# Kernel optimization log

Hardware: AMD Instinct MI355X
Metric: run time of the kernel (lower is better)

The kernel has to match this reference:

```python
import jax, jax.numpy as jnp
import numpy as np

TOPK = 13
NUM_CLASSES = 80
ALPHA = 1.0
BETA = 3.0
EPS = 1e-9
K_NEAR = 4
N_BINS = 36  # theta bins: arange(0, 360, 10)


def _dist_max_per_bin(anc_points, gt_pts):
    """gt_pts: (bs,nm,360,2), anc_points: (na,2) -> (bs,nm,na,36) ray targets."""
    d = gt_pts[:, :, None, :, :] - anc_points[None, None, :, None, :]  # (bs,nm,na,360,2)
    dist = jnp.sqrt(jnp.sum(d * d, axis=-1))                           # (bs,nm,na,360)
    ang = jnp.rad2deg(jnp.arctan2(d[..., 1], d[..., 0])) % 360.0       # (bs,nm,na,360)
    theta = jnp.arange(0, 360, 360 // N_BINS).astype(ang.dtype)        # (36,)

    def per_theta(th):
        diff = jnp.abs(ang - th)
        diff = jnp.where(diff > 180.0, 360.0 - diff, diff)
        neg_v, idx = jax.lax.top_k(-diff, K_NEAR)   # 4 nearest-angle contour pts
        val = -neg_v
        dk = jnp.take_along_axis(dist, idx, axis=-1)
        dk = jnp.where(jnp.min(val, axis=-1, keepdims=True) > 3.0, 1e-6, dk)
        return jnp.max(dk, axis=-1)                 # (bs,nm,na)

    dm = jax.lax.map(per_theta, theta)              # (36,bs,nm,na); chunked to bound memory
    return jnp.maximum(jnp.moveaxis(dm, 0, -1), 1e-6)


def _mask_iou(target, pred):
    l_max = jnp.maximum(target, pred)
    l_min = jnp.maximum(jnp.minimum(target, pred), 1e-6)
    return jnp.sum(l_min, -1) / jnp.sum(l_max, -1)


def _forward(pd_scores, pd_bboxes, anc_points, gt_labels, gt_bboxes, mask_gt, gt_coor):
    bs, na, nc = pd_scores.shape
    nm = gt_bboxes.shape[1]
    gl = gt_labels[..., 0]            # (bs,nm) int
    mgt = mask_gt[..., 0]             # (bs,nm) float
    gt_pts = gt_coor.reshape(bs, nm, 360, 2)

    # select_candidates_in_gts: anchor center strictly inside gt box
    lt, rb = gt_bboxes[..., :2], gt_bboxes[..., 2:]
    deltas = jnp.concatenate([anc_points[None, None] - lt[:, :, None],
                              rb[:, :, None] - anc_points[None, None]], axis=-1)
    mask_in_gts = (jnp.min(deltas, -1) > 1e-9).astype(pd_scores.dtype)  # (bs,nm,na)
    mask_sel = (mask_in_gts * mgt[:, :, None]) > 0

    # get_box_metrics_polar (dense over (bs,nm,na) instead of boolean-mask select)
    dist_max = _dist_max_per_bin(anc_points, gt_pts)                    # (bs,nm,na,36)
    overlaps = jnp.where(mask_sel, _mask_iou(dist_max, pd_bboxes[:, None]), 0.0)
    bbox_scores = jnp.take_along_axis(jnp.swapaxes(pd_scores, 1, 2), gl[:, :, None], axis=1)
    bbox_scores = jnp.where(mask_sel, bbox_scores, 0.0)
    align_metric = (bbox_scores ** ALPHA) * (overlaps ** BETA)

    # select_topk_candidates
    _, topk_idxs = jax.lax.top_k(align_metric, TOPK)
    topk_idxs = jnp.where(mgt[:, :, None] > 0, topk_idxs, 0)
    count = jnp.sum(jax.nn.one_hot(topk_idxs, na, dtype=align_metric.dtype), axis=-2)
    mask_topk = jnp.where(count > 1, 0.0, count)
    mask_pos = mask_topk * mask_in_gts * mgt[:, :, None]

    # select_highest_overlaps
    fg = jnp.sum(mask_pos, -2)                                          # (bs,na)
    multi = fg[:, None, :] > 1
    is_max = jnp.moveaxis(jax.nn.one_hot(jnp.argmax(overlaps, 1), nm, dtype=mask_pos.dtype), -1, 1)
    mask_pos = jnp.where(multi, is_max, mask_pos)
    fg_mask = jnp.sum(mask_pos, -2)
    target_gt_idx = jnp.argmax(mask_pos, -2)                            # (bs,na)

    # per-positive ray-distance targets + polar centerness (dense, masked)
    mask_pos_b = mask_pos > 0
    gt_dist = jnp.where(mask_pos_b[..., None], dist_max, 0.0)           # (bs,nm,na,36)
    cent = jnp.sqrt(jnp.min(dist_max, -1) / jnp.max(dist_max, -1))
    centerness_gt = jnp.where(mask_pos_b, cent, 0.0)                    # (bs,nm,na)

    # get_targets
    target_labels = jnp.maximum(jnp.take_along_axis(gl, target_gt_idx, axis=1), 0)
    target_bboxes = jnp.take_along_axis(gt_bboxes, target_gt_idx[..., None], axis=1)
    target_scores = jax.nn.one_hot(target_labels, NUM_CLASSES, dtype=pd_scores.dtype)
    target_scores = jnp.where((fg_mask > 0)[..., None], target_scores, 0.0)

    am = align_metric * mask_pos
    pos_align = jnp.max(am, -1, keepdims=True)
    pos_ov = jnp.max(overlaps * mask_pos, -1, keepdims=True)
    norm_align = jnp.max(am * pos_ov / (pos_align + EPS), -2)[..., None]  # (bs,na,1)
    target_scores = target_scores * norm_align

    return (target_labels, target_bboxes, target_scores, mask_pos_b,
            target_gt_idx, gt_dist, centerness_gt, fg_mask > 0)


def setup_inputs():
    key = jax.random.key(0)
    k = jax.random.split(key, 6)
    bs, nc, nm = 2, 80, 10
    pts, strs = [], []
    for s in (8, 16, 32):  # 640x640 YOLO grid -> 8400 anchors
        n = 640 // s
        yv, xv = np.meshgrid(np.arange(n), np.arange(n), indexing='ij')
        pts.append(np.stack([(xv + 0.5) * s, (yv + 0.5) * s], -1).reshape(-1, 2))
        strs.append(np.full((pts[-1].shape[0], 1), s, dtype=np.float32))
    anc_points = jnp.asarray(np.concatenate(pts).astype(np.float32))
    stride_tensor = jnp.asarray(np.concatenate(strs))
    na = anc_points.shape[0]
    pd_scores = jax.random.uniform(k[0], (bs, na, nc), dtype=jnp.float32)
    pd_bboxes = jax.random.uniform(k[1], (bs, na, 36), dtype=jnp.float32) * 100.0 + 1.0
    gt_labels = jax.random.randint(k[2], (bs, nm, 1), 0, nc)
    ctr = jax.random.uniform(k[3], (bs, nm, 2), dtype=jnp.float32) * 440.0 + 100.0
    wh = jax.random.uniform(k[4], (bs, nm, 2), dtype=jnp.float32) * 140.0 + 40.0
    gt_bboxes = jnp.concatenate([ctr - wh / 2.0, ctr + wh / 2.0], -1)
    th = jnp.arange(360.0) * (jnp.pi / 180.0)
    rad = (jnp.min(wh, -1, keepdims=True) / 2.0) * (0.6 + 0.4 * jax.random.uniform(k[5], (bs, nm, 360), dtype=jnp.float32))
    ray = jnp.stack([jnp.cos(th), jnp.sin(th)], -1)  # (360,2)
    gt_coor = (ctr[:, :, None, :] + rad[..., None] * ray[None, None]).reshape(bs, nm, 720)
    mask_gt = jnp.ones((bs, nm, 1), dtype=jnp.float32).at[1, 7:].set(0.0)
    return dict(pd_scores=pd_scores, pd_bboxes=pd_bboxes, anc_points=anc_points,
                gt_labels=gt_labels, gt_bboxes=gt_bboxes, mask_gt=mask_gt,
                gt_coor=gt_coor, stride_tensor=stride_tensor, ss=640,
                gt_center=ctr, imgsz=640)


def reference(pd_scores, pd_bboxes, anc_points, gt_labels, gt_bboxes, mask_gt, gt_coor, stride_tensor, ss, gt_center, imgsz):
    # ss, gt_center, imgsz, stride_tensor are accepted (as in the torch signature) but unused
    return _forward(pd_scores, pd_bboxes, anc_points, gt_labels, gt_bboxes, mask_gt, gt_coor)
```

## Files before the change

### kernel.cpp

```cpp
#include <hip/hip_runtime.h>

#define BS 2
#define NM 10
#define NA 8400
#define NC 80
#define NBIN 36
#define KTOP 13
#define NRECT (BS*NM*3)
#define WDIST_CAP 16384

typedef unsigned long long ull;

__device__ __forceinline__ void rect_one(int bm, int lv,
    const float* __restrict__ gtb, const float* __restrict__ mgt,
    int& x0, int& y0, int& cx, int& cy, int& cnt, int& n, int& base){
  cnt = 0; x0 = 0; y0 = 0; cx = 0; cy = 0; n = 0; base = 0;
  if (mgt[bm] > 0.f){
    float s = (float)(8 << lv);
    n = 640 >> (3 + lv);
    base = (lv == 0) ? 0 : ((lv == 1) ? 6400 : 8000);
    float lx = gtb[bm*4+0], ly = gtb[bm*4+1];
    float rx = gtb[bm*4+2], ry = gtb[bm*4+3];
    int a0 = (int)ceilf(lx/s - 0.5f); a0 = min(max(a0, 0), n);
    while (a0 > 0   &&  (((a0-1)+0.5f)*s - lx > 1e-9f)) a0--;
    while (a0 < n   && !(((a0  )+0.5f)*s - lx > 1e-9f)) a0++;
    int a1 = (int)floorf(rx/s - 0.5f); a1 = min(max(a1, -1), n-1);
    while (a1 < n-1 &&  (rx - ((a1+1)+0.5f)*s > 1e-9f)) a1++;
    while (a1 >= 0  && !(rx - ((a1  )+0.5f)*s > 1e-9f)) a1--;
    int b0 = (int)ceilf(ly/s - 0.5f); b0 = min(max(b0, 0), n);
    while (b0 > 0   &&  (((b0-1)+0.5f)*s - ly > 1e-9f)) b0--;
    while (b0 < n   && !(((b0  )+0.5f)*s - ly > 1e-9f)) b0++;
    int b1 = (int)floorf(ry/s - 0.5f); b1 = min(max(b1, -1), n-1);
    while (b1 < n-1 &&  (ry - ((b1+1)+0.5f)*s > 1e-9f)) b1++;
    while (b1 >= 0  && !(ry - ((b1  )+0.5f)*s > 1e-9f)) b1--;
    cx = max(0, a1 - a0 + 1);
    cy = max(0, b1 - b0 + 1);
    cnt = cx * cy;
    x0 = a0; y0 = b0;
  }
}

__device__ __forceinline__ void rect_setup(int tid,
    const float* __restrict__ gtb, const float* __restrict__ mgt,
    int* sx0, int* sy0, int* scx, int* scy, int* scum, int* sn, int* sbase){
  if (tid < NRECT){
    int bm = tid/3, lv = tid - bm*3;
    int x0, y0, cx, cy, cnt, n, base;
    rect_one(bm, lv, gtb, mgt, x0, y0, cx, cy, cnt, n, base);
    sx0[tid] = x0; sy0[tid] = y0; scx[tid] = cx; scy[tid] = cy;
    scum[tid] = cnt; sn[tid] = n; sbase[tid] = base;
  }
  __syncthreads();
  if (tid < 64){
    int c = (tid < NRECT) ? scum[tid] : 0;
    int incl = c;
#pragma unroll
    for (int st = 1; st < 64; st <<= 1){
      int o = __shfl_up(incl, st);
      if (tid >= st) incl += o;
    }
    if (tid < NRECT) scum[tid] = incl - c;
    if (tid == NRECT-1) scum[NRECT] = incl;
  }
  __syncthreads();
}

__device__ __forceinline__ int pair_from_p(int p,
    const int* sx0, const int* sy0, const int* scx,
    const int* scum, const int* sn, const int* sbase){
  int lo = 0, hi = NRECT - 1;
  while (lo < hi){ int mid = (lo + hi + 1) >> 1; if (scum[mid] <= p) lo = mid; else hi = mid - 1; }
  int r = lo;
  int idx = p - scum[r];
  int cx = scx[r];
  int yi = idx / cx;
  int xi = idx - yi*cx;
  int a = sbase[r] + (sy0[r] + yi)*sn[r] + (sx0[r] + xi);
  int bm = r/3;
  return bm*NA + a;
}

__device__ __forceinline__ ull shflx_u64(ull v, int off){
  unsigned lo = (unsigned)v, hi = (unsigned)(v >> 32);
  lo = __shfl_xor(lo, off); hi = __shfl_xor(hi, off);
  return ((ull)hi << 32) | lo;
}

__global__ __launch_bounds__(256)
void k_dist(const float* __restrict__ pds, const float* __restrict__ pdb,
            const float* __restrict__ anc, const int* __restrict__ gl,
            const float* __restrict__ gtb, const float* __restrict__ mgt,
            const float* __restrict__ coor,
            float* __restrict__ out, float* __restrict__ wf){
  float* o_labels  = out;
  float* o_bboxes  = o_labels + BS*NA;
  float* o_scores  = o_bboxes + BS*NA*4;
  float* o_maskpos = o_scores + (size_t)BS*NA*NC;
  float* o_gtidx   = o_maskpos + BS*NM*NA;
  float* o_gtdist  = o_gtidx + BS*NA;
  float* o_cent    = o_gtdist + (size_t)BS*NM*NA*NBIN;
  float* o_fg      = o_cent + BS*NM*NA;

  float* w_align = wf + 16;
  float* w_ovl   = w_align + BS*NM*NA;
  float* w_dist  = w_ovl + BS*NM*NA;

  __shared__ int sx0[NRECT], sy0[NRECT], scx[NRECT], scy[NRECT], scum[NRECT+1], sn[NRECT], sbase[NRECT];
  __shared__ float2 s_ad[360];
  __shared__ unsigned short s_ix[360];
  __shared__ int s_cnt[NBIN], s_off[NBIN+1], s_cur[NBIN];
  __shared__ float s_res[NBIN];
  __shared__ int s_fbl[NBIN];
  __shared__ int s_nfb;

  int tid = threadIdx.x;
  int lane = tid & 63, wave = tid >> 6;

  rect_setup(tid, gtb, mgt, sx0, sy0, scx, scy, scum, sn, sbase);
  int total = scum[NRECT];

  {
    int gtid = blockIdx.x*256 + tid, gsz = gridDim.x*256;
    float4 z4 = make_float4(0.f,0.f,0.f,0.f);
    float4* zs = (float4*)o_scores;
    for (int i = gtid; i < (BS*NA*NC)/4; i += gsz) zs[i] = z4;
    float4* zg = (float4*)o_gtdist;
    for (int i = gtid; i < (BS*NM*NA*NBIN)/4; i += gsz) zg[i] = z4;
    float4* zc = (float4*)o_cent;
    for (int i = gtid; i < (BS*NM*NA)/4; i += gsz) zc[i] = z4;
    float4* zm = (float4*)o_maskpos;
    for (int i = gtid; i < (BS*NM*NA)/4; i += gsz) zm[i] = z4;
    if (gtid < 16) wf[gtid] = 0.f;
    for (int t = gtid; t < BS*NA; t += gsz){
      int b = t / NA;
      o_gtidx[t] = 0.f;
      o_fg[t] = 0.f;
      int lbl = gl[b*NM]; if (lbl < 0) lbl = 0;
      o_labels[t] = (float)lbl;
      const float* bx = gtb + (b*NM)*4;
      ((float4*)o_bboxes)[t] = make_float4(bx[0], bx[1], bx[2], bx[3]);
    }
    for (int row = gtid; row < BS*NM*NA; row += gsz){
      int bm = row / NA;
      int a  = row - bm*NA;
      int lv = (a < 6400) ? 0 : ((a < 8000) ? 1 : 2);
      int ai = a - ((lv == 0) ? 0 : ((lv == 1) ? 6400 : 8000));
      int r = bm*3 + lv;
      bool inrect = false;
      if (scx[r] > 0 && scy[r] > 0){
        int n = sn[r];
        int y = ai / n, x = ai - y*n;
        inrect = (x >= sx0[r] && x < sx0[r]+scx[r] &&
                  y >= sy0[r] && y < sy0[r]+scy[r]);
      }
      if (!inrect) w_ovl[row] = 0.f;
    }
  }

  if (tid < NBIN) s_cnt[tid] = 0;
  if (tid == 0) s_nfb = 0;
  __syncthreads();

  int bin4 = tid >> 2;
  int slot4 = tid & 3;

  for (int p = blockIdx.x; p < total; p += gridDim.x){
    int t = pair_from_p(p, sx0, sy0, scx, scum, sn, sbase);
    int a = t % NA; int bm = t / NA; int b = bm / NM;
    float ax = anc[2*a], ay = anc[2*a+1];
    const float* cc = coor + bm*720;

    float pr = 0.f, sc = 0.f;
    if (wave == 0){
      if (lane < NBIN) pr = pdb[((size_t)b*NA + a)*NBIN + lane];
      int cls = gl[bm];
      sc = pds[((size_t)b*NA + a)*NC + cls];
    }

    float an0, di0, an1 = 0.f, di1 = 0.f;
    int bu0, bu1 = -1;
    {
      float dx = cc[2*tid]   - ax;
      float dy = cc[2*tid+1] - ay;
      di0 = sqrtf(dx*dx + dy*dy);
      an0 = atan2f(dy, dx) * 57.29577951308232f;
      if (an0 < 0.f) an0 += 360.f;
      bu0 = min((int)(an0 * 0.1f), NBIN-1);
      atomicAdd(&s_cnt[bu0], 1);
    }
    if (tid < 104){
      int i = tid + 256;
      float dx = cc[2*i]   - ax;
      float dy = cc[2*i+1] - ay;
      di1 = sqrtf(dx*dx + dy*dy);
      an1 = atan2f(dy, dx) * 57.29577951308232f;
      if (an1 < 0.f) an1 += 360.f;
      bu1 = min((int)(an1 * 0.1f), NBIN-1);
      atomicAdd(&s_cnt[bu1], 1);
    }
    __syncthreads();

    if (wave == 0){
      int c = (lane < NBIN) ? s_cnt[lane] : 0;
      int incl = c;
#pragma unroll
      for (int st = 1; st < 64; st <<= 1){
        int o = __shfl_up(incl, st);
        if (lane >= st) incl += o;
      }
      if (lane < NBIN){ s_off[lane+1] = incl; s_cur[lane] = incl - c; }
      if (lane == 0) s_off[0] = 0;
    }
    __syncthreads();

    if (tid < NBIN) s_cnt[tid] = 0;
    if (tid == 64) s_nfb = 0;
    {
      int pos = atomicAdd(&s_cur[bu0], 1);
      s_ad[pos] = make_float2(an0, di0);
      s_ix[pos] = (unsigned short)tid;
    }
    if (bu1 >= 0){
      int pos = atomicAdd(&s_cur[bu1], 1);
      s_ad[pos] = make_float2(an1, di1);
      s_ix[pos] = (unsigned short)(tid + 256);
    }
    __syncthreads();

#define EVALJ(J, TH) { \
      float2 ad = s_ad[J]; \
      unsigned int ixv = s_ix[J]; \
      float df = fabsf(ad.x - (TH)); \
      df = fminf(df, 360.f - df); \
      ull key = ((ull)__float_as_uint(df) << 32) | ixv; \
      if (key < k3){ \
        k3 = key; d3 = ad.y; \
        if (k3 < k2){ ull tk=k2; k2=k3; k3=tk; float td=d2; d2=d3; d3=td; } \
        if (k2 < k1){ ull tk=k1; k1=k2; k2=tk; float td=d1; d1=d2; d2=td; } \
        if (k1 < k0){ ull tk=k0; k0=k1; k1=tk; float td=d0; d0=d1; d1=td; } \
      } }

    if (bin4 < NBIN){
      float th = (float)(bin4*10);
      int r0s, r0e, r1s, r1e;
      if (bin4 == 0)      { r0s = s_off[35]; r0e = s_off[36]; r1s = 0; r1e = s_off[2]; }
      else if (bin4 == 35){ r0s = s_off[34]; r0e = s_off[36]; r1s = 0; r1e = s_off[1]; }
      else                { r0s = s_off[bin4-1]; r0e = s_off[bin4+2]; r1s = 0; r1e = 0; }
      int L0 = r0e - r0s, L = L0 + (r1e - r1s);
      ull k0,k1,k2,k3; float d0,d1,d2,d3;
      k0=k1=k2=k3=~0ull; d0=d1=d2=d3=0.f;
      for (int w = slot4; w < L; w += 4){
        int j = (w < L0) ? (r0s + w) : (r1s + w - L0);
        EVALJ(j, th)
      }
      float v0m = 0.f, d4v = 0.f, dmax = 0.f;
#pragma unroll
      for (int r = 0; r < 4; r++){
        ull mk = k0; float md = d0;
        ull ok = shflx_u64(mk, 1); float od = __shfl_xor(md, 1);
        if (ok < mk){ mk = ok; md = od; }
        ok = shflx_u64(mk, 2); od = __shfl_xor(md, 2);
        if (ok < mk){ mk = ok; md = od; }
        if (r == 0) v0m = __uint_as_float((unsigned)(mk >> 32));
        if (r == 3) d4v = __uint_as_float((unsigned)(mk >> 32));
        dmax = fmaxf(dmax, md);
        if (k0 == mk){ k0=k1; d0=d1; k1=k2; d1=d2; k2=k3; d2=d3; k3=~0ull; d3=0.f; }
      }
      if (slot4 == 0){
        if (!(v0m <= 3.0f)){
          s_res[bin4] = 1e-6f;
        } else if (!(d4v <= 9.99f)){
          int fi = atomicAdd(&s_nfb, 1);
          s_fbl[fi] = bin4;
        } else {
          s_res[bin4] = fmaxf(dmax, 1e-6f);
        }
      }
    }
    __syncthreads();

    int nfb = s_nfb;
    if (nfb > 0){
      for (int f = wave; f < nfb; f += 4){
        int fb = s_fbl[f];
        float th = (float)(fb*10);
        ull k0,k1,k2,k3; float d0,d1,d2,d3;
        k0=k1=k2=k3=~0ull; d0=d1=d2=d3=0.f;
        for (int j = lane; j < 360; j += 64){
          EVALJ(j, th)
        }
        ull hk = k0; float hd = d0; int hp = 0;
        float dmax = 0.f;
#pragma unroll
        for (int r = 0; r < 4; r++){
          ull mk = hk; float md = hd;
#pragma unroll
          for (int off = 1; off < 64; off <<= 1){
            ull ok = shflx_u64(mk, off);
            float od = __shfl_xor(md, off);
            if (ok < mk){ mk = ok; md = od; }
          }
          if (hk == mk){
            hp++;
            hk = (hp==1)? k1 : (hp==2)? k2 : (hp==3)? k3 : ~0ull;
            hd = (hp==1)? d1 : (hp==2)? d2 : (hp==3)? d3 : 0.f;
          }
          dmax = fmaxf(dmax, md);
        }
        if (lane == 0) s_res[fb] = fmaxf(dmax, 1e-6f);
      }
      __syncthreads();
    }
#undef EVALJ

    if (wave == 0){
      float sum_min = 0.f, sum_max = 0.f;
      if (lane < NBIN){
        float dfin = s_res[lane];
        if (p < WDIST_CAP) w_dist[(size_t)p*NBIN + lane] = dfin;
        sum_max = fmaxf(dfin, pr);
        sum_min = fmaxf(fminf(dfin, pr), 1e-6f);
      }
      for (int off = 32; off > 0; off >>= 1){
        sum_min += __shfl_down(sum_min, off);
        sum_max += __shfl_down(sum_max, off);
      }
      if (lane == 0){
        float ov = sum_min / sum_max;
        w_align[t] = sc * ov * ov * ov;
        w_ovl[t]   = ov;
      }
    }
    __syncthreads();
  }
}

__global__ __launch_bounds__(256)
void k_tail(const float* __restrict__ gtb, const float* __restrict__ mgt,
            const float* __restrict__ w_align, const float* __restrict__ w_ovl,
            const float* __restrict__ w_dist, const int* __restrict__ gl,
            float* __restrict__ o_labels, float* __restrict__ o_bboxes,
            float* __restrict__ o_maskpos, float* __restrict__ o_gtidx,
            float* __restrict__ o_fg,
            float* __restrict__ o_gtdist, float* __restrict__ o_cent,
            float* __restrict__ o_scores,
            int* __restrict__ w_sel, int* __restrict__ done){
  __shared__ int sx0[NRECT], sy0[NRECT], scx[NRECT], scy[NRECT], scum[NRECT+1], sn[NRECT], sbase[NRECT];
  __shared__ float sv[256*KTOP];
  __shared__ int   si[256*KTOP];
  __shared__ float wv4[4];
  __shared__ int   wi4[4];
  __shared__ int   sel[BS*NM*KTOP];
  __shared__ unsigned paB[BS*NM], poB[BS*NM];
  __shared__ int fcnt;
  __shared__ int   fT[BS*NM*KTOP];
  __shared__ int   fA[BS*NM*KTOP];
  __shared__ int   fL[BS*NM*KTOP];
  __shared__ float fV[BS*NM*KTOP];
  __shared__ int sLast;

  int tid = threadIdx.x;
  int lane = tid & 63, wave = tid >> 6;

  rect_setup(tid, gtb, mgt, sx0, sy0, scx, scy, scum, sn, sbase);

  int bm = blockIdx.x;
  {
    const float* al = w_align + (size_t)bm*NA;
    int pbase = scum[bm*3], pm1 = scum[bm*3+1], pm2 = scum[bm*3+2], pend = scum[bm*3+3];

    float v[KTOP]; int ix[KTOP];
#pragma unroll
    for (int j = 0; j < KTOP; j++){ v[j] = -1.f; ix[j] = 0x7fffffff; }
    for (int p = pbase + tid; p < pend; p += 256){
      int r = bm*3 + ((p >= pm1) + (p >= pm2));
      int idx = p - scum[r];
      int cx = scx[r];
      int yi = idx / cx;
      int xi = idx - yi*cx;
      int a = sbase[r] + (sy0[r] + yi)*sn[r] + (sx0[r] + xi);
      float x = al[a];
      if (x > v[KTOP-1]){
        v[KTOP-1] = x; ix[KTOP-1] = a;
#pragma unroll
        for (int j = KTOP-1; j > 0; j--){
          if (v[j] > v[j-1]){
            float tv = v[j-1]; v[j-1] = v[j]; v[j] = tv;
            int   ti = ix[j-1]; ix[j-1] = ix[j]; ix[j] = ti;
          }
        }
      }
    }
#pragma unroll
    for (int j = 0; j < KTOP; j++){ sv[tid*KTOP+j] = v[j]; si[tid*KTOP+j] = ix[j]; }

    int head = 0;
    for (int r = 0; r < KTOP; r++){
      float cv = sv[tid*KTOP + head];
      int   ci = si[tid*KTOP + head];
      float rv = cv; int ri = ci;
      for (int off = 32; off > 0; off >>= 1){
        float ov = __shfl_down(rv, off);
        int   oi = __shfl_down(ri, off);
        if (ov > rv || (ov == rv && oi < ri)){ rv = ov; ri = oi; }
      }
      if (lane == 0){ wv4[wave] = rv; wi4[wave] = ri; }
      __syncthreads();
      float Wv = wv4[0]; int Wi = wi4[0];
#pragma unroll
      for (int w = 1; w < 4; w++){
        float ov = wv4[w]; int oi = wi4[w];
        if (ov > Wv || (ov == Wv && oi < Wi)){ Wv = ov; Wi = oi; }
      }
      if (ci == Wi && head < KTOP-1) head++;
      if (tid == 0)
        __hip_atomic_store(&w_sel[bm*KTOP + r], (Wv > 0.f) ? Wi : -1,
                           __ATOMIC_RELAXED, __HIP_MEMORY_SCOPE_AGENT);
      __syncthreads();
    }
  }

  if (tid == 0){
    __threadfence();
    int old = __hip_atomic_fetch_add(done, 1, __ATOMIC_ACQ_REL, __HIP_MEMORY_SCOPE_AGENT);
    sLast = (old == BS*NM - 1) ? 1 : 0;
  }
  __syncthreads();
  if (!sLast) return;

  for (int s = tid; s < BS*NM*KTOP; s += 256)
    sel[s] = __hip_atomic_load(&w_sel[s], __ATOMIC_RELAXED, __HIP_MEMORY_SCOPE_AGENT);
  if (tid < BS*NM){ paB[tid] = 0u; poB[tid] = 0u; }
  if (tid == 0) fcnt = 0;
  __syncthreads();

  for (int s = tid; s < BS*NM*KTOP; s += 256){
    int a = sel[s];
    if (a >= 0){
      int sbm = s / KTOP;
      int b   = sbm / NM;
      int s0 = b*NM*KTOP;
      int cnt = 0, minS = 1 << 30;
      for (int s2 = s0; s2 < s0 + NM*KTOP; s2++){
        if (sel[s2] == a){ cnt++; if (s2 < minS) minS = s2; }
      }
      if (s == minS){
        int bi = sbm - b*NM;
        if (cnt > 1){
          float bv = -1.f; bi = 0;
#pragma unroll
          for (int mm = 0; mm < NM; mm++){
            float vv = w_ovl[((size_t)(b*NM+mm))*NA + a];
            if (vv > bv){ bv = vv; bi = mm; }
          }
        }
        int bmw = b*NM + bi;
        int ta  = b*NA + a;
        o_maskpos[(size_t)bmw*NA + a] = 1.f;
        o_gtidx[ta] = (float)bi;
        o_fg[ta] = 1.f;
        int lbl = gl[bmw]; if (lbl < 0) lbl = 0;
        o_labels[ta] = (float)lbl;
        const float* bx = gtb + bmw*4;
        ((float4*)o_bboxes)[ta] = make_float4(bx[0], bx[1], bx[2], bx[3]);
        float av  = w_align[(size_t)bmw*NA + a];
        float ovv = w_ovl[(size_t)bmw*NA + a];
        atomicMax(&paB[bmw], __float_as_uint(av));
        atomicMax(&poB[bmw], __float_as_uint(ovv));
        int j = atomicAdd(&fcnt, 1);
        fT[j] = bmw*NA + a; fA[j] = ta; fL[j] = lbl; fV[j] = av;
      }
    }
  }
  __syncthreads();

  int nf = fcnt;
  for (int j = tid; j < nf; j += 256){
    int tf = fT[j];
    int a = tf % NA; int bmw = tf / NA;
    int lv = (a < 6400) ? 0 : ((a < 8000) ? 1 : 2);
    int ai = a - ((lv == 0) ? 0 : ((lv == 1) ? 6400 : 8000));
    int r = bmw*3 + lv;
    int n = sn[r];
    int y = ai / n, x = ai - y*n;
    int p = scum[r] + (y - sy0[r])*scx[r] + (x - sx0[r]);
    const float4* src = (const float4*)(w_dist + (size_t)p*NBIN);
    float4* dst = (float4*)(o_gtdist + (size_t)tf*NBIN);
    float vmin = 1e30f, vmax = 0.f;
#pragma unroll
    for (int q = 0; q < 9; q++){
      float4 v4 = src[q];
      dst[q] = v4;
      vmin = fminf(vmin, fminf(fminf(v4.x, v4.y), fminf(v4.z, v4.w)));
      vmax = fmaxf(vmax, fmaxf(fmaxf(v4.x, v4.y), fmaxf(v4.z, v4.w)));
    }
    o_cent[tf] = sqrtf(vmin / vmax);
    float paf = __uint_as_float(paB[bmw]);
    float pof = __uint_as_float(poB[bmw]);
    o_scores[(size_t)fA[j]*NC + fL[j]] = fV[j] * pof / (paf + 1e-9f);
  }
}

extern "C" void kernel_launch(void* const* d_in, const int* in_sizes, int n_in,
                              void* d_out, int out_size, void* d_ws, size_t ws_size,
                              hipStream_t stream){
  const float* pds  = (const float*)d_in[0];
  const float* pdb  = (const float*)d_in[1];
  const float* anc  = (const float*)d_in[2];
  const int*   gl   = (const int*)  d_in[3];
  const float* gtb  = (const float*)d_in[4];
  const float* mgt  = (const float*)d_in[5];
  const float* coor = (const float*)d_in[6];

  float* out = (float*)d_out;
  float* o_labels  = out;
  float* o_bboxes  = o_labels + BS*NA;
  float* o_scores  = o_bboxes + BS*NA*4;
  float* o_maskpos = o_scores + (size_t)BS*NA*NC;
  float* o_gtidx   = o_maskpos + BS*NM*NA;
  float* o_gtdist  = o_gtidx + BS*NA;
  float* o_cent    = o_gtdist + (size_t)BS*NM*NA*NBIN;
  float* o_fg      = o_cent + BS*NM*NA;

  float* wf      = (float*)d_ws;
  int*   done    = (int*)d_ws;
  float* w_align = wf + 16;
  float* w_ovl   = w_align + BS*NM*NA;
  float* w_dist  = w_ovl + BS*NM*NA;
  int*   w_sel   = (int*)(w_dist + (size_t)WDIST_CAP*NBIN);

  k_dist<<<2048, 256, 0, stream>>>(pds, pdb, anc, gl, gtb, mgt, coor, out, wf);
  k_tail<<<BS*NM, 256, 0, stream>>>(gtb, mgt, w_align, w_ovl, w_dist, gl,
                                    o_labels, o_bboxes, o_maskpos, o_gtidx, o_fg,
                                    o_gtdist, o_cent, o_scores, w_sel, done);
}
```

Before: 154.7 us.

## Shrink k_dist blocks to 128 threads and do per-bin top-4 in one wave

The k_dist kernel moves from 256-thread blocks (2048 of them) to 128-thread blocks (4096 of them). Each thread now computes three contour points instead of up to two. The per-bin nearest-angle top-4 search is done by a single wave with one lane per bin, scanning its neighbouring buckets serially, instead of four lanes per bin merged with shuffles. Fallback bins and the IoU reduction stay inside that wave, which removes s_res and a couple of block barriers. The point index is packed into a float4 in shared memory. The trade-off is lower parallelism within the bin search (serial per-lane scans, and fallbacks processed by one wave) in exchange for fewer syncs and smaller blocks for more occupancy.

New measurement: 164.2 us. +6.1%, slower.

```diff
diff --git a/kernel.cpp b/kernel.cpp
--- a/kernel.cpp
+++ b/kernel.cpp
@@ -86,7 +86,7 @@
   return ((ull)hi << 32) | lo;
 }
 
-__global__ __launch_bounds__(256)
+__global__ __launch_bounds__(128)
 void k_dist(const float* __restrict__ pds, const float* __restrict__ pdb,
             const float* __restrict__ anc, const int* __restrict__ gl,
             const float* __restrict__ gtb, const float* __restrict__ mgt,
@@ -106,10 +106,8 @@
   float* w_dist  = w_ovl + BS*NM*NA;
 
   __shared__ int sx0[NRECT], sy0[NRECT], scx[NRECT], scy[NRECT], scum[NRECT+1], sn[NRECT], sbase[NRECT];
-  __shared__ float2 s_ad[360];
-  __shared__ unsigned short s_ix[360];
+  __shared__ float4 s_ad[360];
   __shared__ int s_cnt[NBIN], s_off[NBIN+1], s_cur[NBIN];
-  __shared__ float s_res[NBIN];
   __shared__ int s_fbl[NBIN];
   __shared__ int s_nfb;
 
@@ -120,7 +118,7 @@
   int total = scum[NRECT];
 
   {
-    int gtid = blockIdx.x*256 + tid, gsz = gridDim.x*256;
+    int gtid = blockIdx.x*128 + tid, gsz = gridDim.x*128;
     float4 z4 = make_float4(0.f,0.f,0.f,0.f);
     float4* zs = (float4*)o_scores;
     for (int i = gtid; i < (BS*NA*NC)/4; i += gsz) zs[i] = z4;
@@ -161,14 +159,11 @@
   if (tid == 0) s_nfb = 0;
   __syncthreads();
 
-  int bin4 = tid >> 2;
-  int slot4 = tid & 3;
-
   for (int p = blockIdx.x; p < total; p += gridDim.x){
     int t = pair_from_p(p, sx0, sy0, scx, scum, sn, sbase);
     int a = t % NA; int bm = t / NA; int b = bm / NM;
     float ax = anc[2*a], ay = anc[2*a+1];
-    const float* cc = coor + bm*720;
+    const float2* cc2 = (const float2*)(coor + bm*720);
 
     float pr = 0.f, sc = 0.f;
     if (wave == 0){
@@ -177,26 +172,23 @@
       sc = pds[((size_t)b*NA + a)*NC + cls];
     }
 
-    float an0, di0, an1 = 0.f, di1 = 0.f;
-    int bu0, bu1 = -1;
-    {
-      float dx = cc[2*tid]   - ax;
-      float dy = cc[2*tid+1] - ay;
-      di0 = sqrtf(dx*dx + dy*dy);
-      an0 = atan2f(dy, dx) * 57.29577951308232f;
-      if (an0 < 0.f) an0 += 360.f;
-      bu0 = min((int)(an0 * 0.1f), NBIN-1);
-      atomicAdd(&s_cnt[bu0], 1);
-    }
-    if (tid < 104){
-      int i = tid + 256;
-      float dx = cc[2*i]   - ax;
-      float dy = cc[2*i+1] - ay;
-      di1 = sqrtf(dx*dx + dy*dy);
-      an1 = atan2f(dy, dx) * 57.29577951308232f;
-      if (an1 < 0.f) an1 += 360.f;
-      bu1 = min((int)(an1 * 0.1f), NBIN-1);
-      atomicAdd(&s_cnt[bu1], 1);
+    float anR[3], diR[3]; int buR[3];
+#pragma unroll
+    for (int r = 0; r < 3; r++){
+      int i = tid + r*128;
+      buR[r] = -1;
+      if (i < 360){
+        float2 cxy = cc2[i];
+        float dx = cxy.x - ax;
+        float dy = cxy.y - ay;
+        diR[r] = sqrtf(dx*dx + dy*dy);
+        float an = atan2f(dy, dx) * 57.29577951308232f;
+        if (an < 0.f) an += 360.f;
+        anR[r] = an;
+        int bu = min((int)(an * 0.1f), NBIN-1);
+        buR[r] = bu;
+        atomicAdd(&s_cnt[bu], 1);
+      }
     }
     __syncthreads();
 
@@ -214,22 +206,18 @@
     __syncthreads();
 
     if (tid < NBIN) s_cnt[tid] = 0;
-    if (tid == 64) s_nfb = 0;
-    {
-      int pos = atomicAdd(&s_cur[bu0], 1);
-      s_ad[pos] = make_float2(an0, di0);
-      s_ix[pos] = (unsigned short)tid;
-    }
-    if (bu1 >= 0){
-      int pos = atomicAdd(&s_cur[bu1], 1);
-      s_ad[pos] = make_float2(an1, di1);
-      s_ix[pos] = (unsigned short)(tid + 256);
+#pragma unroll
+    for (int r = 0; r < 3; r++){
+      if (buR[r] >= 0){
+        int pos = atomicAdd(&s_cur[buR[r]], 1);
+        s_ad[pos] = make_float4(anR[r], diR[r], (float)(tid + r*128), 0.f);
+      }
     }
     __syncthreads();
 
 #define EVALJ(J, TH) { \
-      float2 ad = s_ad[J]; \
-      unsigned int ixv = s_ix[J]; \
+      float4 ad = s_ad[J]; \
+      unsigned int ixv = (unsigned int)(int)ad.z; \
       float df = fabsf(ad.x - (TH)); \
       df = fminf(df, 360.f - df); \
       ull key = ((ull)__float_as_uint(df) << 32) | ixv; \
@@ -240,48 +228,34 @@
         if (k1 < k0){ ull tk=k0; k0=k1; k1=tk; float td=d0; d0=d1; d1=td; } \
       } }
 
-    if (bin4 < NBIN){
-      float th = (float)(bin4*10);
-      int r0s, r0e, r1s, r1e;
-      if (bin4 == 0)      { r0s = s_off[35]; r0e = s_off[36]; r1s = 0; r1e = s_off[2]; }
-      else if (bin4 == 35){ r0s = s_off[34]; r0e = s_off[36]; r1s = 0; r1e = s_off[1]; }
-      else                { r0s = s_off[bin4-1]; r0e = s_off[bin4+2]; r1s = 0; r1e = 0; }
-      int L0 = r0e - r0s, L = L0 + (r1e - r1s);
-      ull k0,k1,k2,k3; float d0,d1,d2,d3;
-      k0=k1=k2=k3=~0ull; d0=d1=d2=d3=0.f;
-      for (int w = slot4; w < L; w += 4){
-        int j = (w < L0) ? (r0s + w) : (r1s + w - L0);
-        EVALJ(j, th)
-      }
-      float v0m = 0.f, d4v = 0.f, dmax = 0.f;
-#pragma unroll
-      for (int r = 0; r < 4; r++){
-        ull mk = k0; float md = d0;
-        ull ok = shflx_u64(mk, 1); float od = __shfl_xor(md, 1);
-        if (ok < mk){ mk = ok; md = od; }
-        ok = shflx_u64(mk, 2); od = __shfl_xor(md, 2);
-        if (ok < mk){ mk = ok; md = od; }
-        if (r == 0) v0m = __uint_as_float((unsigned)(mk >> 32));
-        if (r == 3) d4v = __uint_as_float((unsigned)(mk >> 32));
-        dmax = fmaxf(dmax, md);
-        if (k0 == mk){ k0=k1; d0=d1; k1=k2; d1=d2; k2=k3; d2=d3; k3=~0ull; d3=0.f; }
-      }
-      if (slot4 == 0){
+    if (wave == 0){
+      float dfin = 1e-6f;
+      bool act = (lane < NBIN);
+      bool need_fb = false;
+      if (act){
+        float th = (float)(lane*10);
+        int r0s, r0e, r1s, r1e;
+        if (lane == 0)      { r0s = s_off[35]; r0e = s_off[36]; r1s = 0; r1e = s_off[2]; }
+        else if (lane == 35){ r0s = s_off[34]; r0e = s_off[36]; r1s = 0; r1e = s_off[1]; }
+        else                { r0s = s_off[lane-1]; r0e = s_off[lane+2]; r1s = 0; r1e = 0; }
+        ull k0,k1,k2,k3; float d0,d1,d2,d3;
+        k0=k1=k2=k3=~0ull; d0=d1=d2=d3=0.f;
+        for (int j = r0s; j < r0e; j++) EVALJ(j, th)
+        for (int j = r1s; j < r1e; j++) EVALJ(j, th)
+        float v0m = __uint_as_float((unsigned)(k0 >> 32));
+        float d4v = __uint_as_float((unsigned)(k3 >> 32));
         if (!(v0m <= 3.0f)){
-          s_res[bin4] = 1e-6f;
+          dfin = 1e-6f;
         } else if (!(d4v <= 9.99f)){
           int fi = atomicAdd(&s_nfb, 1);
-          s_fbl[fi] = bin4;
+          s_fbl[fi] = lane;
+          need_fb = true;
         } else {
-          s_res[bin4] = fmaxf(dmax, 1e-6f);
+          dfin = fmaxf(fmaxf(fmaxf(d0,d1),fmaxf(d2,d3)), 1e-6f);
         }
       }
-    }
-    __syncthreads();
-
-    int nfb = s_nfb;
-    if (nfb > 0){
-      for (int f = wave; f < nfb; f += 4){
+      int nfb = s_nfb;
+      for (int f = 0; f < nfb; f++){
         int fb = s_fbl[f];
         float th = (float)(fb*10);
         ull k0,k1,k2,k3; float d0,d1,d2,d3;
@@ -307,16 +281,12 @@
           }
           dmax = fmaxf(dmax, md);
         }
-        if (lane == 0) s_res[fb] = fmaxf(dmax, 1e-6f);
-      }
-      __syncthreads();
-    }
-#undef EVALJ
-
-    if (wave == 0){
+        if (lane == fb && need_fb) dfin = fmaxf(dmax, 1e-6f);
+      }
+      if (lane == 0) s_nfb = 0;
+
       float sum_min = 0.f, sum_max = 0.f;
-      if (lane < NBIN){
-        float dfin = s_res[lane];
+      if (act){
         if (p < WDIST_CAP) w_dist[(size_t)p*NBIN + lane] = dfin;
         sum_max = fmaxf(dfin, pr);
         sum_min = fmaxf(fminf(dfin, pr), 1e-6f);
@@ -331,6 +301,7 @@
         w_ovl[t]   = ov;
       }
     }
+#undef EVALJ
     __syncthreads();
   }
 }
@@ -529,7 +500,7 @@
   float* w_dist  = w_ovl + BS*NM*NA;
   int*   w_sel   = (int*)(w_dist + (size_t)WDIST_CAP*NBIN);
 
-  k_dist<<<2048, 256, 0, stream>>>(pds, pdb, anc, gl, gtb, mgt, coor, out, wf);
+  k_dist<<<4096, 128, 0, stream>>>(pds, pdb, anc, gl, gtb, mgt, coor, out, wf);
   k_tail<<<BS*NM, 256, 0, stream>>>(gtb, mgt, w_align, w_ovl, w_dist, gl,
                                     o_labels, o_bboxes, o_maskpos, o_gtidx, o_fg,
                                     o_gtdist, o_cent, o_scores, w_sel, done);
```
